# Kernel tuning notes

Measured on AMD Instinct MI355X. Metric: run time of the kernel, lower is better.

## Reference

```python
import jax, jax.numpy as jnp
import numpy as np

N_HEAD = 16
ROPE_BASE = 10000.0


def _rope_cache(T, head_dim):
    # half-split RoPE: cos/sin of shape [T, head_dim//2]
    half = head_dim // 2
    inv_freq = ROPE_BASE ** (-jnp.arange(half, dtype=jnp.float32) / half)
    angles = jnp.arange(T, dtype=jnp.float32)[:, None] * inv_freq[None, :]  # [T, half]
    return jnp.cos(angles), jnp.sin(angles)


def _apply_rope(x, cos, sin):
    # x: [B, H, T, D]; cos/sin: [T, D//2]
    half = x.shape[-1] // 2
    x1, x2 = x[..., :half], x[..., half:]
    c = cos[None, None, :, :]
    s = sin[None, None, :, :]
    return jnp.concatenate([x1 * c - x2 * s, x1 * s + x2 * c], axis=-1)


def setup_inputs() -> dict:
    key = jax.random.key(0)
    k1, k2, k3 = jax.random.split(key, 3)
    B, T, C = 2, 2048, 1024
    x = jax.random.normal(k1, (B, T, C), dtype=jnp.float32)
    w_attn = jax.random.normal(k2, (C, 3 * C), dtype=jnp.float32) * (C ** -0.5)
    b_attn = jnp.zeros((3 * C,), dtype=jnp.float32)
    w_proj = jax.random.normal(k3, (C, C), dtype=jnp.float32) * (C ** -0.5)
    b_proj = jnp.zeros((C,), dtype=jnp.float32)
    return {"x": x, "w_attn": w_attn, "b_attn": b_attn, "w_proj": w_proj, "b_proj": b_proj}


def reference(x, w_attn, b_attn, w_proj, b_proj):
    B, T, C = x.shape
    H = N_HEAD
    hd = C // H

    qkv = x @ w_attn + b_attn                      # [B, T, 3C] fused QKV
    q, k, v = jnp.split(qkv, 3, axis=-1)
    q = q.reshape(B, T, H, hd).transpose(0, 2, 1, 3)  # [B, H, T, hd]
    k = k.reshape(B, T, H, hd).transpose(0, 2, 1, 3)
    v = v.reshape(B, T, H, hd).transpose(0, 2, 1, 3)

    cos, sin = _rope_cache(T, hd)
    q = _apply_rope(q, cos, sin)
    k = _apply_rope(k, cos, sin)

    scale = 1.0 / jnp.sqrt(jnp.float32(hd))
    att = jnp.einsum("bhqd,bhkd->bhqk", q, k) * scale  # [B, H, T, T]
    causal = jnp.tril(jnp.ones((T, T), dtype=bool))
    att = jnp.where(causal[None, None], att, -jnp.inf)
    att = jax.nn.softmax(att, axis=-1)
    y = jnp.einsum("bhqk,bhkd->bhqd", att, v)          # [B, H, T, hd]
    y = y.transpose(0, 2, 1, 3).reshape(B, T, C)
    return y @ w_proj + b_proj
```

## Files before the change

kernel.cpp:

```cpp
#include <hip/hip_runtime.h>
#include <hip/hip_bf16.h>
#include <cmath>

typedef _Float16 half_t;
typedef half_t half4 __attribute__((ext_vector_type(4)));
typedef half_t half8 __attribute__((ext_vector_type(8)));
typedef float f32x4 __attribute__((ext_vector_type(4)));

#define N_HEADS 16
#define HD      64
#define T_SEQ   2048
#define B_SZ    2
#define C_DIM   1024
#define M_ROWS  (B_SZ * T_SEQ)
#define N_QKV   (3 * C_DIM)
#define QSCALE  0.18033688f

__device__ inline void load_lds16(const half_t* g, half_t* l) {
  __builtin_amdgcn_global_load_lds(
      (const __attribute__((address_space(1))) void*)g,
      (__attribute__((address_space(3))) void*)l, 16, 0, 0);
}

__global__ __launch_bounds__(256) void k_prep(const float* __restrict__ x,
                                              half_t* __restrict__ xb,
                                              const float* __restrict__ wa,
                                              half_t* __restrict__ wT,
                                              const float* __restrict__ wp,
                                              half_t* __restrict__ wpT) {
  __shared__ float tile[64][65];
  int bid = blockIdx.x, tid = threadIdx.x;
  if (bid < 4096) {
    int i = (bid * 256 + tid) * 4;
    float4 v = *(const float4*)(x + i);
    half_t o[4] = {(half_t)v.x, (half_t)v.y, (half_t)v.z, (half_t)v.w};
    *(ulong1*)(xb + i) = *(ulong1*)o;
    return;
  }
  const float* in; half_t* out; int K, N, id;
  if (bid < 4096 + 768) { id = bid - 4096; in = wa; out = wT;  K = 1024; N = 3072; }
  else                  { id = bid - 4864; in = wp; out = wpT; K = 1024; N = 1024; }
  int n0 = (id % (N / 64)) * 64, k0 = (id / (N / 64)) * 64;
  int tx = tid & 63, ty = tid >> 6;
  #pragma unroll
  for (int i = 0; i < 64; i += 4)
    tile[ty + i][tx] = in[(size_t)(k0 + ty + i) * N + n0 + tx];
  __syncthreads();
  #pragma unroll
  for (int i = 0; i < 64; i += 4) {
    int r = ty + i;
    out[(size_t)(n0 + r) * K + k0 + tx] = (half_t)tile[tx][r];
  }
}

template <typename OT, int TN>
__global__ __launch_bounds__(256) void k_gemm(const half_t* __restrict__ A,
                                              const half_t* __restrict__ Bt,
                                              const float* __restrict__ bias,
                                              OT* __restrict__ C,
                                              int M, int N, int K) {
  constexpr int NI = TN / 32;
  __shared__ half_t As[128 * 64];
  __shared__ half_t Bs[TN * 64];
  int tid = threadIdx.x;
  int wave = tid >> 6, lane = tid & 63;
  int lane15 = lane & 15, quad = lane >> 4;
  int wm = (wave >> 1) * 64, wn = (wave & 1) * (TN / 2);
  int bm0 = blockIdx.y * 128, bn0 = blockIdx.x * TN;
  f32x4 acc[4][NI] = {};

  for (int kb = 0; kb < K; kb += 64) {
    const half_t* Ag = A + (size_t)bm0 * K + kb;
    const half_t* Bg = Bt + (size_t)bn0 * K + kb;
    __syncthreads();
    #pragma unroll
    for (int p = 0; p < 4; p++) {
      int fc = wave * 4 * 64 + p * 64 + lane;
      int r = fc >> 3, c = (fc & 7) ^ (r & 7);
      load_lds16(Ag + (size_t)r * K + c * 8, As + (wave * 4 + p) * 512);
    }
    #pragma unroll
    for (int p = 0; p < NI; p++) {
      int fc = wave * NI * 64 + p * 64 + lane;
      int r = fc >> 3, c = (fc & 7) ^ (r & 7);
      load_lds16(Bg + (size_t)r * K + c * 8, Bs + (wave * NI + p) * 512);
    }
    __syncthreads();
    #pragma unroll
    for (int ks = 0; ks < 2; ks++) {
      half8 af[4], bf[NI];
      #pragma unroll
      for (int i = 0; i < 4; i++) {
        int Ra = wm + i * 16 + lane15;
        af[i] = *(const half8*)(As + Ra * 64 + ((ks * 4 + quad) ^ (Ra & 7)) * 8);
      }
      #pragma unroll
      for (int i = 0; i < NI; i++) {
        int Rb = wn + i * 16 + lane15;
        bf[i] = *(const half8*)(Bs + Rb * 64 + ((ks * 4 + quad) ^ (Rb & 7)) * 8);
      }
      #pragma unroll
      for (int mi = 0; mi < 4; mi++)
        #pragma unroll
        for (int ni = 0; ni < NI; ni++)
          acc[mi][ni] = __builtin_amdgcn_mfma_f32_16x16x32_f16(af[mi], bf[ni], acc[mi][ni], 0, 0, 0);
    }
  }
  #pragma unroll
  for (int mi = 0; mi < 4; mi++)
    #pragma unroll
    for (int ni = 0; ni < NI; ni++) {
      int n = bn0 + wn + ni * 16 + lane15;
      float bv = bias[n];
      int mrow = bm0 + wm + mi * 16 + quad * 4;
      #pragma unroll
      for (int r = 0; r < 4; r++)
        C[(size_t)(mrow + r) * N + n] = (OT)(acc[mi][ni][r] + bv);
    }
}

__global__ __launch_bounds__(256) void k_rope(const half_t* __restrict__ qkv,
                                              half_t* __restrict__ Q,
                                              half_t* __restrict__ Ko,
                                              half_t* __restrict__ Vt) {
  __shared__ float vt[64][65];
  int bh = blockIdx.y;
  int b = bh >> 4, h = bh & 15;
  int t0 = blockIdx.x * 64;
  int tid = threadIdx.x;
  int trow = tid >> 5, i = tid & 31;
  float inv = exp2f(-(float)i * (13.287712379549449f / 32.0f));
  #pragma unroll
  for (int p = 0; p < 8; p++) {
    int tloc = p * 8 + trow;
    int t = t0 + tloc;
    const half_t* row = qkv + (size_t)(b * T_SEQ + t) * N_QKV;
    float q1 = (float)row[h * 64 + i],        q2 = (float)row[h * 64 + i + 32];
    float k1 = (float)row[1024 + h * 64 + i], k2 = (float)row[1024 + h * 64 + i + 32];
    float v1 = (float)row[2048 + h * 64 + i], v2 = (float)row[2048 + h * 64 + i + 32];
    float s, c;
    sincosf((float)t * inv, &s, &c);
    size_t base = ((size_t)bh * T_SEQ + t) * HD;
    Q[base + i]       = (half_t)((q1 * c - q2 * s) * QSCALE);
    Q[base + i + 32]  = (half_t)((q1 * s + q2 * c) * QSCALE);
    Ko[base + i]      = (half_t)(k1 * c - k2 * s);
    Ko[base + i + 32] = (half_t)(k1 * s + k2 * c);
    vt[i][tloc]      = v1;
    vt[i + 32][tloc] = v2;
  }
  __syncthreads();
  int d = tid >> 6, tc = tid & 63;
  #pragma unroll
  for (int p = 0; p < 16; p++) {
    int dd = p * 4 + d;
    Vt[((size_t)bh * HD + dd) * T_SEQ + t0 + tc] = (half_t)vt[dd][tc];
  }
}

__global__ __launch_bounds__(256) void k_flash(const half_t* __restrict__ Qg,
                                               const half_t* __restrict__ Kg,
                                               const half_t* __restrict__ Vg,
                                               half_t* __restrict__ y) {
  __shared__ union {
    struct { half_t K[2][4096]; half_t V[2][4096]; } s;
    struct { float O[4][32][65]; float L[4][64]; } r;
  } u;
  int bh = blockIdx.y;
  int b = bh >> 4, h = bh & 15;
  int tid = threadIdx.x;
  int wave = tid >> 6, lane = tid & 63;
  int lane15 = lane & 15, quad = lane >> 4;
  const half_t* Qb = Qg + (size_t)bh * T_SEQ * HD;
  const half_t* Kb = Kg + (size_t)bh * T_SEQ * HD;
  const half_t* Vb = Vg + (size_t)bh * HD * T_SEQ;
  const half4 ones = {(half_t)1.f, (half_t)1.f, (half_t)1.f, (half_t)1.f};

  int Rk = wave * 16 + lane15;
  int kOff0 = (Rk * 8 + ((quad) ^ (Rk & 7))) * 8;
  int kOff1 = (Rk * 8 + ((4 + quad) ^ (Rk & 7))) * 8;
  int vcc = wave * 2 + (quad >> 1);
  int vOff[4];
  #pragma unroll
  for (int nm = 0; nm < 4; nm++) {
    int Rv = nm * 16 + lane15;
    vOff[nm] = (Rv * 8 + (vcc ^ (Rv & 7))) * 8 + (quad & 1) * 4;
  }

  #define STAGE(buf, kv0)                                                      \
    {                                                                          \
      _Pragma("unroll")                                                        \
      for (int pp = 0; pp < 2; pp++) {                                         \
        int fc = (wave * 2 + pp) * 64 + lane;                                  \
        int rr = fc >> 3, cc = (fc & 7) ^ (rr & 7);                            \
        load_lds16(Kb + (size_t)((kv0) + rr) * HD + cc * 8,                    \
                   &u.s.K[buf][0] + fc * 8);                                   \
        load_lds16(Vb + (size_t)rr * T_SEQ + (kv0) + cc * 8,                   \
                   &u.s.V[buf][0] + fc * 8);                                   \
      }                                                                        \
    }

  #pragma unroll
  for (int phase = 0; phase < 2; phase++) {
    int qt = phase == 0 ? (int)blockIdx.x : (31 - (int)blockIdx.x);
    int q0 = qt * 64;
    half8 bq[4][2];
    #pragma unroll
    for (int qf = 0; qf < 4; qf++) {
      const half_t* qp = Qb + (size_t)(q0 + qf * 16 + lane15) * HD;
      bq[qf][0] = *(const half8*)(qp + quad * 8);
      bq[qf][1] = *(const half8*)(qp + 32 + quad * 8);
    }
    f32x4 ot[4][4] = {};
    f32x4 lacc[4] = {};

    STAGE(0, 0);
    for (int j = 0; j < qt; j++) {
      int buf = j & 1;
      __syncthreads();
      STAGE(buf ^ 1, (j + 1) * 64);
      const half_t* Kt = &u.s.K[buf][0];
      const half_t* Vt = &u.s.V[buf][0];
      half8 ak0 = *(const half8*)(Kt + kOff0);
      half8 ak1 = *(const half8*)(Kt + kOff1);
      f32x4 sacc[4];
      #pragma unroll
      for (int qf = 0; qf < 4; qf++) {
        f32x4 z = {};
        z = __builtin_amdgcn_mfma_f32_16x16x32_f16(ak0, bq[qf][0], z, 0, 0, 0);
        sacc[qf] = __builtin_amdgcn_mfma_f32_16x16x32_f16(ak1, bq[qf][1], z, 0, 0, 0);
      }
      half4 bp[4];
      #pragma unroll
      for (int qf = 0; qf < 4; qf++) {
        #pragma unroll
        for (int r = 0; r < 4; r++)
          bp[qf][r] = (half_t)exp2f(fminf(sacc[qf][r], 14.0f));
        lacc[qf] = __builtin_amdgcn_mfma_f32_16x16x16f16(ones, bp[qf], lacc[qf], 0, 0, 0);
      }
      #pragma unroll
      for (int nm = 0; nm < 4; nm++) {
        half4 av = *(const half4*)(Vt + vOff[nm]);
        #pragma unroll
        for (int qf = 0; qf < 4; qf++)
          ot[nm][qf] = __builtin_amdgcn_mfma_f32_16x16x16f16(av, bp[qf], ot[nm][qf], 0, 0, 0);
      }
    }

    {
      int buf = qt & 1;
      __syncthreads();
      const half_t* Kt = &u.s.K[buf][0];
      const half_t* Vt = &u.s.V[buf][0];
      half8 ak0 = *(const half8*)(Kt + kOff0);
      half8 ak1 = *(const half8*)(Kt + kOff1);
      f32x4 sacc[4];
      #pragma unroll
      for (int qf = 0; qf < 4; qf++) {
        f32x4 z = {};
        z = __builtin_amdgcn_mfma_f32_16x16x32_f16(ak0, bq[qf][0], z, 0, 0, 0);
        sacc[qf] = __builtin_amdgcn_mfma_f32_16x16x32_f16(ak1, bq[qf][1], z, 0, 0, 0);
      }
      half4 bp[4];
      #pragma unroll
      for (int qf = 0; qf < 4; qf++) {
        #pragma unroll
        for (int r = 0; r < 4; r++) {
          float sv = sacc[qf][r];
          if (wave * 16 + quad * 4 + r > qf * 16 + lane15) sv = -1.0e30f;
          bp[qf][r] = (half_t)exp2f(fminf(sv, 14.0f));
        }
        lacc[qf] = __builtin_amdgcn_mfma_f32_16x16x16f16(ones, bp[qf], lacc[qf], 0, 0, 0);
      }
      #pragma unroll
      for (int nm = 0; nm < 4; nm++) {
        half4 av = *(const half4*)(Vt + vOff[nm]);
        #pragma unroll
        for (int qf = 0; qf < 4; qf++)
          ot[nm][qf] = __builtin_amdgcn_mfma_f32_16x16x16f16(av, bp[qf], ot[nm][qf], 0, 0, 0);
      }
    }
    __syncthreads();

    int ql = tid >> 2, dg = (tid & 3) * 8;
    float invl = 0.f;
    #pragma unroll
    for (int hf = 0; hf < 2; hf++) {
      #pragma unroll
      for (int nm2 = 0; nm2 < 2; nm2++) {
        int nm = hf * 2 + nm2;
        #pragma unroll
        for (int qf = 0; qf < 4; qf++)
          #pragma unroll
          for (int r = 0; r < 4; r++)
            u.r.O[wave][nm2 * 16 + quad * 4 + r][qf * 16 + lane15] = ot[nm][qf][r];
      }
      if (hf == 0) {
        #pragma unroll
        for (int qf = 0; qf < 4; qf++)
          u.r.L[wave][qf * 16 + lane15] = lacc[qf][0];
      }
      __syncthreads();
      if (hf == 0)
        invl = 1.0f / (u.r.L[0][ql] + u.r.L[1][ql] + u.r.L[2][ql] + u.r.L[3][ql]);
      half8 o8;
      #pragma unroll
      for (int dd = 0; dd < 8; dd++) {
        float s = u.r.O[0][dg + dd][ql] + u.r.O[1][dg + dd][ql] +
                  u.r.O[2][dg + dd][ql] + u.r.O[3][dg + dd][ql];
        o8[dd] = (half_t)(s * invl);
      }
      *(half8*)(y + (size_t)(b * T_SEQ + q0 + ql) * C_DIM + h * 64 + hf * 32 + dg) = o8;
      __syncthreads();
    }
  }
  #undef STAGE
}

extern "C" void kernel_launch(void* const* d_in, const int* in_sizes, int n_in,
                              void* d_out, int out_size, void* d_ws, size_t ws_size,
                              hipStream_t stream) {
  const float* x      = (const float*)d_in[0];
  const float* w_attn = (const float*)d_in[1];
  const float* b_attn = (const float*)d_in[2];
  const float* w_proj = (const float*)d_in[3];
  const float* b_proj = (const float*)d_in[4];
  float* out = (float*)d_out;

  char* ws = (char*)d_ws;
  const size_t MB = 1u << 20;
  half_t* xb  = (half_t*)(ws);
  half_t* wT  = (half_t*)(ws + 8 * MB);
  half_t* wpT = (half_t*)(ws + 14 * MB);
  half_t* Q   = (half_t*)(ws + 16 * MB);
  half_t* Kb  = (half_t*)(ws + 24 * MB);
  half_t* Vt  = (half_t*)(ws + 32 * MB);
  half_t* qkv = (half_t*)(ws + 40 * MB);
  half_t* y   = (half_t*)(ws + 40 * MB);

  k_prep<<<4096 + 768 + 256, 256, 0, stream>>>(x, xb, w_attn, wT, w_proj, wpT);
  k_gemm<half_t, 128><<<dim3(N_QKV / 128, M_ROWS / 128), 256, 0, stream>>>(
      xb, wT, b_attn, qkv, M_ROWS, N_QKV, C_DIM);
  k_rope<<<dim3(T_SEQ / 64, B_SZ * N_HEADS), 256, 0, stream>>>(qkv, Q, Kb, Vt);
  k_flash<<<dim3(16, B_SZ * N_HEADS), 256, 0, stream>>>(Q, Kb, Vt, y);
  k_gemm<float, 64><<<dim3(C_DIM / 64, M_ROWS / 128), 256, 0, stream>>>(
      y, wpT, b_proj, out, M_ROWS, C_DIM, C_DIM);
}
```

Baseline: 204.5 us.

## Split flash work per query tile and give each wave its own query rows

The flash kernel now launches one block per 64-row query tile instead of pairing two tiles per block, with a remapped blockIdx-to-tile order meant to balance causal work. Before, the four waves split the key dimension and then reduced partial outputs through LDS. Now each wave owns 16 query rows across all keys, so that cross-wave LDS reduction and its extra barriers go away. The row sum is kept in a scalar and reduced with shuffles. The cost is that each wave reads the full K/V tile from LDS, and per-block work is now uneven across the grid.

```diff
diff --git a/kernel.cpp b/kernel.cpp
--- a/kernel.cpp
+++ b/kernel.cpp
@@ -161,30 +161,19 @@
                                                const half_t* __restrict__ Kg,
                                                const half_t* __restrict__ Vg,
                                                half_t* __restrict__ y) {
-  __shared__ union {
-    struct { half_t K[2][4096]; half_t V[2][4096]; } s;
-    struct { float O[4][32][65]; float L[4][64]; } r;
-  } u;
+  __shared__ half_t Ks[2][4096];
+  __shared__ half_t Vs[2][4096];
   int bh = blockIdx.y;
   int b = bh >> 4, h = bh & 15;
+  int x = blockIdx.x, g = x & 7, m = x >> 3;
+  int qt = (m == 0) ? 2 * g : (m == 1) ? 2 * g + 1
+         : (m == 2) ? 31 - 2 * g : 30 - 2 * g;
   int tid = threadIdx.x;
   int wave = tid >> 6, lane = tid & 63;
   int lane15 = lane & 15, quad = lane >> 4;
   const half_t* Qb = Qg + (size_t)bh * T_SEQ * HD;
   const half_t* Kb = Kg + (size_t)bh * T_SEQ * HD;
   const half_t* Vb = Vg + (size_t)bh * HD * T_SEQ;
-  const half4 ones = {(half_t)1.f, (half_t)1.f, (half_t)1.f, (half_t)1.f};
-
-  int Rk = wave * 16 + lane15;
-  int kOff0 = (Rk * 8 + ((quad) ^ (Rk & 7))) * 8;
-  int kOff1 = (Rk * 8 + ((4 + quad) ^ (Rk & 7))) * 8;
-  int vcc = wave * 2 + (quad >> 1);
-  int vOff[4];
-  #pragma unroll
-  for (int nm = 0; nm < 4; nm++) {
-    int Rv = nm * 16 + lane15;
-    vOff[nm] = (Rv * 8 + (vcc ^ (Rv & 7))) * 8 + (quad & 1) * 4;
-  }
 
   #define STAGE(buf, kv0)                                                      \
     {                                                                          \
@@ -193,125 +182,103 @@
         int fc = (wave * 2 + pp) * 64 + lane;                                  \
         int rr = fc >> 3, cc = (fc & 7) ^ (rr & 7);                            \
         load_lds16(Kb + (size_t)((kv0) + rr) * HD + cc * 8,                    \
-                   &u.s.K[buf][0] + fc * 8);                                   \
+                   &Ks[buf][0] + fc * 8);                                      \
         load_lds16(Vb + (size_t)rr * T_SEQ + (kv0) + cc * 8,                   \
-                   &u.s.V[buf][0] + fc * 8);                                   \
+                   &Vs[buf][0] + fc * 8);                                      \
       }                                                                        \
     }
 
-  #pragma unroll
-  for (int phase = 0; phase < 2; phase++) {
-    int qt = phase == 0 ? (int)blockIdx.x : (31 - (int)blockIdx.x);
-    int q0 = qt * 64;
-    half8 bq[4][2];
-    #pragma unroll
-    for (int qf = 0; qf < 4; qf++) {
-      const half_t* qp = Qb + (size_t)(q0 + qf * 16 + lane15) * HD;
-      bq[qf][0] = *(const half8*)(qp + quad * 8);
-      bq[qf][1] = *(const half8*)(qp + 32 + quad * 8);
-    }
-    f32x4 ot[4][4] = {};
-    f32x4 lacc[4] = {};
-
-    STAGE(0, 0);
-    for (int j = 0; j < qt; j++) {
-      int buf = j & 1;
-      __syncthreads();
-      STAGE(buf ^ 1, (j + 1) * 64);
-      const half_t* Kt = &u.s.K[buf][0];
-      const half_t* Vt = &u.s.V[buf][0];
-      half8 ak0 = *(const half8*)(Kt + kOff0);
-      half8 ak1 = *(const half8*)(Kt + kOff1);
-      f32x4 sacc[4];
-      #pragma unroll
-      for (int qf = 0; qf < 4; qf++) {
-        f32x4 z = {};
-        z = __builtin_amdgcn_mfma_f32_16x16x32_f16(ak0, bq[qf][0], z, 0, 0, 0);
-        sacc[qf] = __builtin_amdgcn_mfma_f32_16x16x32_f16(ak1, bq[qf][1], z, 0, 0, 0);
-      }
-      half4 bp[4];
-      #pragma unroll
-      for (int qf = 0; qf < 4; qf++) {
-        #pragma unroll
-        for (int r = 0; r < 4; r++)
-          bp[qf][r] = (half_t)exp2f(fminf(sacc[qf][r], 14.0f));
-        lacc[qf] = __builtin_amdgcn_mfma_f32_16x16x16f16(ones, bp[qf], lacc[qf], 0, 0, 0);
+  int q0 = qt * 64;
+  int qrow = q0 + wave * 16 + lane15;
+  half8 bq0 = *(const half8*)(Qb + (size_t)qrow * HD + quad * 8);
+  half8 bq1 = *(const half8*)(Qb + (size_t)qrow * HD + 32 + quad * 8);
+  f32x4 ot[4] = {};
+  float l = 0.f;
+
+  STAGE(0, 0);
+  for (int j = 0; j < qt; j++) {
+    int buf = j & 1;
+    __syncthreads();
+    STAGE(buf ^ 1, (j + 1) * 64);
+    const half_t* Kt = &Ks[buf][0];
+    const half_t* Vt = &Vs[buf][0];
+    f32x4 sacc[4];
+    #pragma unroll
+    for (int s = 0; s < 4; s++) {
+      int R = s * 16 + lane15;
+      half8 ak0 = *(const half8*)(Kt + R * 64 + ((quad) ^ (R & 7)) * 8);
+      half8 ak1 = *(const half8*)(Kt + R * 64 + ((4 + quad) ^ (R & 7)) * 8);
+      f32x4 z = {};
+      z = __builtin_amdgcn_mfma_f32_16x16x32_f16(ak0, bq0, z, 0, 0, 0);
+      sacc[s] = __builtin_amdgcn_mfma_f32_16x16x32_f16(ak1, bq1, z, 0, 0, 0);
+    }
+    #pragma unroll
+    for (int s = 0; s < 4; s++) {
+      half4 bp;
+      #pragma unroll
+      for (int r = 0; r < 4; r++) {
+        float p = exp2f(fminf(sacc[s][r], 14.0f));
+        l += p;
+        bp[r] = (half_t)p;
       }
       #pragma unroll
       for (int nm = 0; nm < 4; nm++) {
-        half4 av = *(const half4*)(Vt + vOff[nm]);
-        #pragma unroll
-        for (int qf = 0; qf < 4; qf++)
-          ot[nm][qf] = __builtin_amdgcn_mfma_f32_16x16x16f16(av, bp[qf], ot[nm][qf], 0, 0, 0);
-      }
-    }
-
-    {
-      int buf = qt & 1;
-      __syncthreads();
-      const half_t* Kt = &u.s.K[buf][0];
-      const half_t* Vt = &u.s.V[buf][0];
-      half8 ak0 = *(const half8*)(Kt + kOff0);
-      half8 ak1 = *(const half8*)(Kt + kOff1);
-      f32x4 sacc[4];
-      #pragma unroll
-      for (int qf = 0; qf < 4; qf++) {
-        f32x4 z = {};
-        z = __builtin_amdgcn_mfma_f32_16x16x32_f16(ak0, bq[qf][0], z, 0, 0, 0);
-        sacc[qf] = __builtin_amdgcn_mfma_f32_16x16x32_f16(ak1, bq[qf][1], z, 0, 0, 0);
-      }
-      half4 bp[4];
-      #pragma unroll
-      for (int qf = 0; qf < 4; qf++) {
-        #pragma unroll
-        for (int r = 0; r < 4; r++) {
-          float sv = sacc[qf][r];
-          if (wave * 16 + quad * 4 + r > qf * 16 + lane15) sv = -1.0e30f;
-          bp[qf][r] = (half_t)exp2f(fminf(sv, 14.0f));
-        }
-        lacc[qf] = __builtin_amdgcn_mfma_f32_16x16x16f16(ones, bp[qf], lacc[qf], 0, 0, 0);
+        int Rv = nm * 16 + lane15;
+        half4 av = *(const half4*)(Vt + Rv * 64 +
+                                   ((2 * s + (quad >> 1)) ^ (Rv & 7)) * 8 +
+                                   (quad & 1) * 4);
+        ot[nm] = __builtin_amdgcn_mfma_f32_16x16x16f16(av, bp, ot[nm], 0, 0, 0);
+      }
+    }
+  }
+  {
+    int buf = qt & 1;
+    __syncthreads();
+    const half_t* Kt = &Ks[buf][0];
+    const half_t* Vt = &Vs[buf][0];
+    f32x4 sacc[4];
+    #pragma unroll
+    for (int s = 0; s < 4; s++) {
+      int R = s * 16 + lane15;
+      half8 ak0 = *(const half8*)(Kt + R * 64 + ((quad) ^ (R & 7)) * 8);
+      half8 ak1 = *(const half8*)(Kt + R * 64 + ((4 + quad) ^ (R & 7)) * 8);
+      f32x4 z = {};
+      z = __builtin_amdgcn_mfma_f32_16x16x32_f16(ak0, bq0, z, 0, 0, 0);
+      sacc[s] = __builtin_amdgcn_mfma_f32_16x16x32_f16(ak1, bq1, z, 0, 0, 0);
+    }
+    #pragma unroll
+    for (int s = 0; s < 4; s++) {
+      half4 bp;
+      #pragma unroll
+      for (int r = 0; r < 4; r++) {
+        float sv = sacc[s][r];
+        if (s * 16 + quad * 4 + r > wave * 16 + lane15) sv = -1.0e30f;
+        float p = exp2f(fminf(sv, 14.0f));
+        l += p;
+        bp[r] = (half_t)p;
       }
       #pragma unroll
       for (int nm = 0; nm < 4; nm++) {
-        half4 av = *(const half4*)(Vt + vOff[nm]);
-        #pragma unroll
-        for (int qf = 0; qf < 4; qf++)
-          ot[nm][qf] = __builtin_amdgcn_mfma_f32_16x16x16f16(av, bp[qf], ot[nm][qf], 0, 0, 0);
-      }
-    }
-    __syncthreads();
-
-    int ql = tid >> 2, dg = (tid & 3) * 8;
-    float invl = 0.f;
-    #pragma unroll
-    for (int hf = 0; hf < 2; hf++) {
-      #pragma unroll
-      for (int nm2 = 0; nm2 < 2; nm2++) {
-        int nm = hf * 2 + nm2;
-        #pragma unroll
-        for (int qf = 0; qf < 4; qf++)
-          #pragma unroll
-          for (int r = 0; r < 4; r++)
-            u.r.O[wave][nm2 * 16 + quad * 4 + r][qf * 16 + lane15] = ot[nm][qf][r];
-      }
-      if (hf == 0) {
-        #pragma unroll
-        for (int qf = 0; qf < 4; qf++)
-          u.r.L[wave][qf * 16 + lane15] = lacc[qf][0];
-      }
-      __syncthreads();
-      if (hf == 0)
-        invl = 1.0f / (u.r.L[0][ql] + u.r.L[1][ql] + u.r.L[2][ql] + u.r.L[3][ql]);
-      half8 o8;
-      #pragma unroll
-      for (int dd = 0; dd < 8; dd++) {
-        float s = u.r.O[0][dg + dd][ql] + u.r.O[1][dg + dd][ql] +
-                  u.r.O[2][dg + dd][ql] + u.r.O[3][dg + dd][ql];
-        o8[dd] = (half_t)(s * invl);
-      }
-      *(half8*)(y + (size_t)(b * T_SEQ + q0 + ql) * C_DIM + h * 64 + hf * 32 + dg) = o8;
-      __syncthreads();
-    }
+        int Rv = nm * 16 + lane15;
+        half4 av = *(const half4*)(Vt + Rv * 64 +
+                                   ((2 * s + (quad >> 1)) ^ (Rv & 7)) * 8 +
+                                   (quad & 1) * 4);
+        ot[nm] = __builtin_amdgcn_mfma_f32_16x16x16f16(av, bp, ot[nm], 0, 0, 0);
+      }
+    }
+  }
+
+  l += __shfl_xor(l, 16);
+  l += __shfl_xor(l, 32);
+  float invl = 1.0f / l;
+  int t = q0 + wave * 16 + lane15;
+  half_t* yr = y + (size_t)(b * T_SEQ + t) * C_DIM + h * 64;
+  #pragma unroll
+  for (int nm = 0; nm < 4; nm++) {
+    half4 o4;
+    #pragma unroll
+    for (int r = 0; r < 4; r++) o4[r] = (half_t)(ot[nm][r] * invl);
+    *(half4*)(yr + nm * 16 + quad * 4) = o4;
   }
   #undef STAGE
 }
@@ -341,7 +308,7 @@
   k_gemm<half_t, 128><<<dim3(N_QKV / 128, M_ROWS / 128), 256, 0, stream>>>(
       xb, wT, b_attn, qkv, M_ROWS, N_QKV, C_DIM);
   k_rope<<<dim3(T_SEQ / 64, B_SZ * N_HEADS), 256, 0, stream>>>(qkv, Q, Kb, Vt);
-  k_flash<<<dim3(16, B_SZ * N_HEADS), 256, 0, stream>>>(Q, Kb, Vt, y);
+  k_flash<<<dim3(32, B_SZ * N_HEADS), 256, 0, stream>>>(Q, Kb, Vt, y);
   k_gemm<float, 64><<<dim3(C_DIM / 64, M_ROWS / 128), 256, 0, stream>>>(
       y, wpT, b_proj, out, M_ROWS, C_DIM, C_DIM);
 }
```

New measurement: 217.0 us. +6.1%, slower.
